# Optimization experiments

Hardware: AMD Instinct MI355X
Metric: run time of the kernel (lower is better)

## Reference

```python
import jax, jax.numpy as jnp
import numpy as np

N_EXPERTS = 48
N_CATEGORIES = 30
SPATIAL = (24, 28, 20)  # img_size // 4


def apply_topk_sparsity(x, K_select):
    """Top-K over expert dim (dim 0) by |value|; others zeroed. x: (k,c,X,Y,Z)."""
    n = x.shape[0]
    # move expert axis last and flatten voxels: (M, n)
    xt = jnp.moveaxis(x, 0, -1).reshape(-1, n)
    _, idx = jax.lax.top_k(jnp.abs(xt), K_select)  # (M, K)
    rows = jnp.arange(xt.shape[0])[:, None]
    mask = jnp.zeros_like(xt).at[rows, idx].set(1.0)
    g = xt * mask
    g = g.reshape(x.shape[1:] + (n,))
    return jnp.moveaxis(g, -1, 0)


def setup_inputs() -> dict:
    key = jax.random.key(0)
    k1, k2, k3 = jax.random.split(key, 3)
    shp = (N_EXPERTS, N_CATEGORIES) + SPATIAL
    return {
        "gating_m": jax.random.normal(k1, shp, dtype=jnp.float32),
        "gating_f": jax.random.normal(k2, shp, dtype=jnp.float32),
        "shape_experts": jax.random.normal(k3, shp, dtype=jnp.float32),
        "k_experts": 24,
    }


def reference(gating_m, gating_f, shape_experts, k_experts):
    sparse_m = apply_topk_sparsity(gating_m, k_experts)
    sparse_f = apply_topk_sparsity(gating_f, k_experts)
    # gated combination of spatial expert codebooks: contract expert dim
    Im_map = jnp.einsum('kcxyz,kcxyz->cxyz', sparse_m, shape_experts)
    If_map = jnp.einsum('kcxyz,kcxyz->cxyz', sparse_f, shape_experts)
    Im_seg = jax.nn.softmax(Im_map, axis=0)[None]  # (1,c,X,Y,Z)
    If_seg = jax.nn.softmax(If_map, axis=0)[None]
    return jnp.stack([Im_seg, If_seg])  # (2,1,c,X,Y,Z)
```

## Files before the change

kernel.cpp:

```cpp
#include <hip/hip_runtime.h>
#include <math.h>
#include <stdint.h>

#define NEXP 48
#define NCAT 30
#define SP_TOT 13440
#define M_TOT (NCAT * SP_TOT)
#define COLS_PER_BLOCK 32
#define PADK 49

__global__ __launch_bounds__(256) void moe_topk_contract(
    const float* __restrict__ gm, const float* __restrict__ gf,
    const float* __restrict__ se, const int* __restrict__ kptr,
    float* __restrict__ out)
{
    __shared__ uint64_t keys[COLS_PER_BLOCK * PADK];
    __shared__ float    gval[COLS_PER_BLOCK * PADK];

    const int tid       = threadIdx.x;
    const int colbase   = blockIdx.x * COLS_PER_BLOCK;
    const int col_local = tid >> 3;
    const int sub       = tid & 7;
    const int col       = colbase + col_local;
    const int K         = *kptr;

    float se_own[6];
    #pragma unroll
    for (int ii = 0; ii < 6; ++ii)
        se_own[ii] = se[(sub * 6 + ii) * M_TOT + col];

    #pragma unroll 1
    for (int t = 0; t < 2; ++t) {
        const float* __restrict__ g_ = t ? gf : gm;

        #pragma unroll
        for (int rep = 0; rep < 6; ++rep) {
            const int e = rep * 8 + (tid >> 5);
            const int c = tid & 31;
            const float v = g_[e * M_TOT + colbase + c];
            const uint32_t ab = __float_as_uint(v) & 0x7fffffffu;
            keys[c * PADK + e] = ((uint64_t)ab << 32) | (uint32_t)(NEXP - 1 - e);
            gval[c * PADK + e] = v;
        }
        __syncthreads();

        uint64_t kown[6];
        float    gown[6];
        int      r[6];
        #pragma unroll
        for (int ii = 0; ii < 6; ++ii) {
            kown[ii] = keys[col_local * PADK + sub * 6 + ii];
            gown[ii] = gval[col_local * PADK + sub * 6 + ii];
            r[ii] = 0;
        }

        #pragma unroll
        for (int j = 0; j < NEXP; ++j) {
            const uint64_t kj = keys[col_local * PADK + j];
            #pragma unroll
            for (int ii = 0; ii < 6; ++ii)
                r[ii] += (kj > kown[ii]) ? 1 : 0;
        }

        float acc = 0.f;
        #pragma unroll
        for (int ii = 0; ii < 6; ++ii)
            acc = (r[ii] < K) ? fmaf(gown[ii], se_own[ii], acc) : acc;

        acc += __shfl_xor(acc, 1);
        acc += __shfl_xor(acc, 2);
        acc += __shfl_xor(acc, 4);
        if (sub == 0) out[t * M_TOT + col] = acc;
        __syncthreads();
    }
}

__global__ __launch_bounds__(256) void softmax_c(float* __restrict__ out)
{
    const int q = blockIdx.x * blockDim.x + threadIdx.x;
    if (q >= 2 * SP_TOT) return;
    const int t  = q / SP_TOT;
    const int sp = q - t * SP_TOT;
    float* __restrict__ base = out + t * M_TOT + sp;

    float v[NCAT];
    float mx = -INFINITY;
    #pragma unroll
    for (int c = 0; c < NCAT; ++c) {
        v[c] = base[c * SP_TOT];
        mx = fmaxf(mx, v[c]);
    }
    float sum = 0.f;
    #pragma unroll
    for (int c = 0; c < NCAT; ++c) {
        v[c] = __expf(v[c] - mx);
        sum += v[c];
    }
    const float inv = 1.f / sum;
    #pragma unroll
    for (int c = 0; c < NCAT; ++c)
        base[c * SP_TOT] = v[c] * inv;
}

extern "C" void kernel_launch(void* const* d_in, const int* in_sizes, int n_in,
                              void* d_out, int out_size, void* d_ws, size_t ws_size,
                              hipStream_t stream) {
    const float* gm   = (const float*)d_in[0];
    const float* gf   = (const float*)d_in[1];
    const float* se   = (const float*)d_in[2];
    const int*   kptr = (const int*)d_in[3];
    float* out = (float*)d_out;

    const int grid1 = M_TOT / COLS_PER_BLOCK;
    moe_topk_contract<<<grid1, 256, 0, stream>>>(gm, gf, se, kptr, out);

    const int grid2 = (2 * SP_TOT + 255) / 256;
    softmax_c<<<grid2, 256, 0, stream>>>(out);
}
```

Measured before the change: 119.3 us.

## Rank experts with float compares and fall back to 64-bit keys only on ties

```diff
diff --git a/kernel.cpp b/kernel.cpp
--- a/kernel.cpp
+++ b/kernel.cpp
@@ -6,28 +6,25 @@
 #define NCAT 30
 #define SP_TOT 13440
 #define M_TOT (NCAT * SP_TOT)
-#define COLS_PER_BLOCK 32
-#define PADK 49
+#define CPB 64
+#define PAD 52
 
 __global__ __launch_bounds__(256) void moe_topk_contract(
     const float* __restrict__ gm, const float* __restrict__ gf,
     const float* __restrict__ se, const int* __restrict__ kptr,
     float* __restrict__ out)
 {
-    __shared__ uint64_t keys[COLS_PER_BLOCK * PADK];
-    __shared__ float    gval[COLS_PER_BLOCK * PADK];
+    __shared__ __align__(16) float gv[CPB * PAD];
 
     const int tid       = threadIdx.x;
-    const int colbase   = blockIdx.x * COLS_PER_BLOCK;
+    const int colbase   = blockIdx.x * CPB;
     const int col_local = tid >> 3;
     const int sub       = tid & 7;
-    const int col       = colbase + col_local;
+    const int cA        = col_local;
+    const int cB        = col_local + 32;
+    const int colA      = colbase + cA;
+    const int colB      = colbase + cB;
     const int K         = *kptr;
-
-    float se_own[6];
-    #pragma unroll
-    for (int ii = 0; ii < 6; ++ii)
-        se_own[ii] = se[(sub * 6 + ii) * M_TOT + col];
 
     #pragma unroll 1
     for (int t = 0; t < 2; ++t) {
@@ -35,42 +32,93 @@
 
         #pragma unroll
         for (int rep = 0; rep < 6; ++rep) {
-            const int e = rep * 8 + (tid >> 5);
-            const int c = tid & 31;
-            const float v = g_[e * M_TOT + colbase + c];
-            const uint32_t ab = __float_as_uint(v) & 0x7fffffffu;
-            keys[c * PADK + e] = ((uint64_t)ab << 32) | (uint32_t)(NEXP - 1 - e);
-            gval[c * PADK + e] = v;
+            const int e2 = rep * 8 + (tid >> 6) * 2;
+            const int c  = tid & 63;
+            const float v0 = g_[e2 * M_TOT + colbase + c];
+            const float v1 = g_[(e2 + 1) * M_TOT + colbase + c];
+            *(float2*)&gv[c * PAD + e2] = make_float2(v0, v1);
         }
         __syncthreads();
 
-        uint64_t kown[6];
-        float    gown[6];
-        int      r[6];
+        float gA[6], gB[6];
+        #pragma unroll
+        for (int p = 0; p < 3; ++p) {
+            const float2 a = *(const float2*)&gv[cA * PAD + sub * 6 + p * 2];
+            const float2 b = *(const float2*)&gv[cB * PAD + sub * 6 + p * 2];
+            gA[p * 2] = a.x; gA[p * 2 + 1] = a.y;
+            gB[p * 2] = b.x; gB[p * 2 + 1] = b.y;
+        }
+
+        int rA[6] = {0, 0, 0, 0, 0, 0};
+        int rB[6] = {0, 0, 0, 0, 0, 0};
+        #pragma unroll
+        for (int j4 = 0; j4 < 12; ++j4) {
+            const float4 qa = *(const float4*)&gv[cA * PAD + j4 * 4];
+            const float4 qb = *(const float4*)&gv[cB * PAD + j4 * 4];
+            const float ja[4] = {qa.x, qa.y, qa.z, qa.w};
+            const float jb[4] = {qb.x, qb.y, qb.z, qb.w};
+            #pragma unroll
+            for (int u = 0; u < 4; ++u) {
+                #pragma unroll
+                for (int ii = 0; ii < 6; ++ii) {
+                    rA[ii] += (fabsf(ja[u]) > fabsf(gA[ii]));
+                    rB[ii] += (fabsf(jb[u]) > fabsf(gB[ii]));
+                }
+            }
+        }
+
+        float seA[6], seB[6];
         #pragma unroll
         for (int ii = 0; ii < 6; ++ii) {
-            kown[ii] = keys[col_local * PADK + sub * 6 + ii];
-            gown[ii] = gval[col_local * PADK + sub * 6 + ii];
-            r[ii] = 0;
+            seA[ii] = se[(sub * 6 + ii) * M_TOT + colA];
+            seB[ii] = se[(sub * 6 + ii) * M_TOT + colB];
         }
 
-        #pragma unroll
-        for (int j = 0; j < NEXP; ++j) {
-            const uint64_t kj = keys[col_local * PADK + j];
+        int SA = rA[0] + rA[1] + rA[2] + rA[3] + rA[4] + rA[5];
+        int SB = rB[0] + rB[1] + rB[2] + rB[3] + rB[4] + rB[5];
+        SA += __shfl_xor(SA, 1); SA += __shfl_xor(SA, 2); SA += __shfl_xor(SA, 4);
+        SB += __shfl_xor(SB, 1); SB += __shfl_xor(SB, 2); SB += __shfl_xor(SB, 4);
+        const bool tie = (SA != 1128) | (SB != 1128);
+
+        if (__any(tie)) {
+            uint64_t kA[6], kB[6];
             #pragma unroll
-            for (int ii = 0; ii < 6; ++ii)
-                r[ii] += (kj > kown[ii]) ? 1 : 0;
+            for (int ii = 0; ii < 6; ++ii) {
+                const uint32_t e = sub * 6 + ii;
+                kA[ii] = ((uint64_t)(__float_as_uint(gA[ii]) & 0x7fffffffu) << 32)
+                         | (uint32_t)(NEXP - 1 - e);
+                kB[ii] = ((uint64_t)(__float_as_uint(gB[ii]) & 0x7fffffffu) << 32)
+                         | (uint32_t)(NEXP - 1 - e);
+                rA[ii] = 0; rB[ii] = 0;
+            }
+            #pragma unroll 1
+            for (int j = 0; j < NEXP; ++j) {
+                const uint64_t kja =
+                    ((uint64_t)(__float_as_uint(gv[cA * PAD + j]) & 0x7fffffffu) << 32)
+                    | (uint32_t)(NEXP - 1 - j);
+                const uint64_t kjb =
+                    ((uint64_t)(__float_as_uint(gv[cB * PAD + j]) & 0x7fffffffu) << 32)
+                    | (uint32_t)(NEXP - 1 - j);
+                #pragma unroll
+                for (int ii = 0; ii < 6; ++ii) {
+                    rA[ii] += (kja > kA[ii]);
+                    rB[ii] += (kjb > kB[ii]);
+                }
+            }
         }
 
-        float acc = 0.f;
+        float accA = 0.f, accB = 0.f;
         #pragma unroll
-        for (int ii = 0; ii < 6; ++ii)
-            acc = (r[ii] < K) ? fmaf(gown[ii], se_own[ii], acc) : acc;
-
-        acc += __shfl_xor(acc, 1);
-        acc += __shfl_xor(acc, 2);
-        acc += __shfl_xor(acc, 4);
-        if (sub == 0) out[t * M_TOT + col] = acc;
+        for (int ii = 0; ii < 6; ++ii) {
+            accA = (rA[ii] < K) ? fmaf(gA[ii], seA[ii], accA) : accA;
+            accB = (rB[ii] < K) ? fmaf(gB[ii], seB[ii], accB) : accB;
+        }
+        accA += __shfl_xor(accA, 1); accA += __shfl_xor(accA, 2); accA += __shfl_xor(accA, 4);
+        accB += __shfl_xor(accB, 1); accB += __shfl_xor(accB, 2); accB += __shfl_xor(accB, 4);
+        if (sub == 0) {
+            out[t * M_TOT + colA] = accA;
+            out[t * M_TOT + colB] = accB;
+        }
         __syncthreads();
     }
 }
@@ -111,7 +159,7 @@
     const int*   kptr = (const int*)d_in[3];
     float* out = (float*)d_out;
 
-    const int grid1 = M_TOT / COLS_PER_BLOCK;
+    const int grid1 = M_TOT / CPB;
     moe_topk_contract<<<grid1, 256, 0, stream>>>(gm, gf, se, kptr, out);
 
     const int grid2 = (2 * SP_TOT + 255) / 256;
```

Measured after the change: 121.0 us. Within noise of the previous version (+1.4%).
